# Kernel optimization log

Measured on AMD Instinct MI355X. Metric: run time of the kernel, lower is better.

Reference implementation:

```python
import jax, jax.numpy as jnp
import numpy as np

N_NODES = 100000
EPS = 1e-12  # F.normalize eps


def _sage_conv(x, src, dst, deg, Wl, bl, Wr):
    # mean aggregation of neighbor (source) features at destination nodes
    agg = jax.ops.segment_sum(x[src], dst, num_segments=N_NODES)  # [N, F]
    agg = agg / jnp.maximum(deg, 1.0)[:, None]
    out = agg @ Wl + bl + x @ Wr  # lin_l(mean(x_j)) + lin_r(x_i)
    # normalize=True -> L2 row normalization
    norm = jnp.sqrt(jnp.sum(out * out, axis=-1, keepdims=True))
    return out / jnp.maximum(norm, EPS)


def setup_inputs() -> dict:
    key = jax.random.key(0)
    ks = jax.random.split(key, 10)
    F_IN, H, C = 14, 32, 2
    x = jax.random.normal(ks[0], (N_NODES, F_IN), dtype=jnp.float32)
    edge_index = jax.random.randint(ks[1], (2, 6400000), 0, N_NODES, dtype=jnp.int32)
    def glorot(k, shape):
        lim = float(np.sqrt(6.0 / (shape[0] + shape[1])))
        return jax.random.uniform(k, shape, jnp.float32, -lim, lim)
    return {
        "x": x,
        "edge_index": edge_index,
        "W1l": glorot(ks[2], (F_IN, H)), "b1": jnp.zeros((H,), jnp.float32),
        "W1r": glorot(ks[3], (F_IN, H)),
        "W2l": glorot(ks[4], (H, H)), "b2": jnp.zeros((H,), jnp.float32),
        "W2r": glorot(ks[5], (H, H)),
        "Wlin": glorot(ks[6], (H, C)), "blin": jnp.zeros((C,), jnp.float32),
    }


def reference(x, edge_index, W1l, b1, W1r, W2l, b2, W2r, Wlin, blin):
    src, dst = edge_index[0], edge_index[1]
    deg = jax.ops.segment_sum(jnp.ones_like(dst, dtype=x.dtype), dst,
                              num_segments=N_NODES)  # in-degree per node
    h = jax.nn.relu(_sage_conv(x, src, dst, deg, W1l, b1, W1r))
    # dropout p=0.2 is identity at inference
    h = jax.nn.relu(_sage_conv(h, src, dst, deg, W2l, b2, W2r))
    return h @ Wlin + blin  # [N, num_classes]
```

## Files before the change

kernel.cpp:

```cpp
#include <hip/hip_runtime.h>
#include <hip/hip_bf16.h>


#define CHA 16384
#define MAXB 512
#define CAPB 18432
#define CAPH 9728
#define NPB 128

static __device__ __forceinline__ unsigned short f2bf(float f) {
    unsigned u = __float_as_uint(f);
    unsigned r = (u + 0x7FFFu + ((u >> 16) & 1u)) >> 16;
    return (unsigned short)r;
}
#define BF_LO(u) __uint_as_float((u) << 16)
#define BF_HI(u) __uint_as_float((u) & 0xFFFF0000u)

__global__ void cvt_x_bf16(const float* __restrict__ x, unsigned short* __restrict__ xb,
                           int* __restrict__ bcursor, int N, int NB) {
    int idx = blockIdx.x * blockDim.x + threadIdx.x;
    if (idx < NB) bcursor[idx] = idx * CAPB;
    if (idx >= N * 16) return;
    int n = idx >> 4, f = idx & 15;
    float v = (f < 14) ? x[n * 14 + f] : 0.f;
    xb[idx] = f2bf(v);
}

__global__ __launch_bounds__(1024) void partitionA(
        const int* __restrict__ src, const int* __restrict__ dst,
        int* __restrict__ bcursor, unsigned* __restrict__ part, int E, int NB) {
    __shared__ unsigned pk[CHA];
    __shared__ int h[MAXB], lofs[MAXB], cur[MAXB], delta[MAXB], tmp[MAXB];
    int t = threadIdx.x;
    int base = blockIdx.x * CHA;
    int end = base + CHA; if (end > E) end = E;
    int cnt = end - base;

    int ed[16], es[16];
    for (int i = t; i < NB; i += 1024) h[i] = 0;
    __syncthreads();
    #pragma unroll
    for (int i = 0; i < 4; ++i) {
        int j = i * 4096 + t * 4;
        if (j + 4 <= cnt) {
            int4 d4 = *(const int4*)(dst + base + j);
            int4 s4 = *(const int4*)(src + base + j);
            ed[i*4+0] = d4.x; ed[i*4+1] = d4.y; ed[i*4+2] = d4.z; ed[i*4+3] = d4.w;
            es[i*4+0] = s4.x; es[i*4+1] = s4.y; es[i*4+2] = s4.z; es[i*4+3] = s4.w;
            atomicAdd(&h[d4.x >> 8], 1);
            atomicAdd(&h[d4.y >> 8], 1);
            atomicAdd(&h[d4.z >> 8], 1);
            atomicAdd(&h[d4.w >> 8], 1);
        } else {
            #pragma unroll
            for (int k = 0; k < 4; ++k) {
                if (j + k < cnt) {
                    ed[i*4+k] = dst[base + j + k];
                    es[i*4+k] = src[base + j + k];
                    atomicAdd(&h[ed[i*4+k] >> 8], 1);
                } else ed[i*4+k] = -1;
            }
        }
    }
    __syncthreads();
    int v = 0;
    if (t < MAXB) { v = (t < NB) ? h[t] : 0; tmp[t] = v; }
    __syncthreads();
    for (int off = 1; off < MAXB; off <<= 1) {
        int a = 0;
        if (t < MAXB && t >= off) a = tmp[t - off];
        __syncthreads();
        if (t < MAXB) tmp[t] += a;
        __syncthreads();
    }
    if (t < NB) {
        int excl = tmp[t] - v;
        lofs[t] = excl;
        cur[t] = excl;
        int g = v ? atomicAdd(&bcursor[t], v) : 0;
        delta[t] = g - excl;
    }
    __syncthreads();
    #pragma unroll
    for (int i = 0; i < 16; ++i) {
        int d = ed[i];
        if (d >= 0) {
            int b = d >> 8;
            int r = atomicAdd(&cur[b], 1);
            pk[r] = ((unsigned)(d & 255) << 24) | (unsigned)es[i];
        }
    }
    __syncthreads();
    int wid = t >> 6, lane = t & 63;
    for (int b = wid; b < NB; b += 16) {
        int s = lofs[b];
        int e2 = (b + 1 < NB) ? lofs[b + 1] : cnt;
        int dlt = delta[b];
        int lim = (b + 1) * CAPB;
        for (int k = s + lane; k < e2; k += 64) {
            int gidx = dlt + k;
            if (gidx < lim) part[gidx] = pk[k];
        }
    }
}

__global__ __launch_bounds__(1024) void partitionB_fused(
        const unsigned* __restrict__ part, const int* __restrict__ bcursor,
        const uint4* __restrict__ xb4, const float* __restrict__ x,
        const float* __restrict__ W1l, const float* __restrict__ b1,
        const float* __restrict__ W1r,
        int* __restrict__ deg, int* __restrict__ offs, int* __restrict__ nlo,
        int* __restrict__ sorted_src, float* __restrict__ hbuf,
        unsigned short* __restrict__ hb, int N, int HALF) {
    __shared__ int pk2[CAPH];
    __shared__ int hh[256], tmp[256], keyofs[256];
    __shared__ int lstart[128], ldeg[128];
    __shared__ float sagg[128 * 17];
    __shared__ float sx[128 * 14];
    __shared__ float swl[448], swr[448], sb1[32];
    __shared__ int sTot;
    int b = blockIdx.x >> 1;
    int halfId = blockIdx.x & 1;
    int t = threadIdx.x;
    int start = b * CAPB;
    int end = bcursor[b];
    if (end > start + CAPB) end = start + CAPB;
    int rbase = blockIdx.x * CAPH;
    unsigned ce[18];
    if (t < 256) hh[t] = 0;
    if (t >= 512 && t < 960) { swl[t - 512] = W1l[t - 512]; swr[t - 512] = W1r[t - 512]; }
    else if (t >= 960 && t < 992) sb1[t - 960] = b1[t - 960];
    __syncthreads();
    #pragma unroll
    for (int i = 0; i < 18; ++i) {
        int idx = start + t + i * 1024;
        unsigned p = 0xFFFFFFFFu;
        if (idx < end) {
            p = part[idx];
            int dl = (int)(p >> 24);
            if ((dl >> 7) == halfId) {
                int key = (dl & 127) * 2 + (((int)(p & 0xFFFFFFu) < HALF) ? 0 : 1);
                atomicAdd(&hh[key], 1);
            } else p = 0xFFFFFFFFu;
        }
        ce[i] = p;
    }
    {
        int nbase = b * 256 + halfId * 128;
        int nnod = N - nbase; if (nnod > 128) nnod = 128; if (nnod < 0) nnod = 0;
        const float* gx = x + (size_t)nbase * 14;
        for (int i = t; i < nnod * 14; i += 1024) sx[i] = gx[i];
    }
    __syncthreads();
    int v = (t < 256) ? hh[t] : 0;
    if (t < 256) tmp[t] = v;
    __syncthreads();
    for (int off = 1; off < 256; off <<= 1) {
        int a2 = (t < 256 && t >= off) ? tmp[t - off] : 0;
        __syncthreads();
        if (t < 256) tmp[t] += a2;
        __syncthreads();
    }
    if (t < 256) keyofs[t] = tmp[t] - v;
    if (t == 255) sTot = tmp[255];
    __syncthreads();
    if (t < 128) {
        int lo = hh[2 * t];
        int d = lo + hh[2 * t + 1];
        int excl = keyofs[2 * t];
        lstart[t] = excl;
        ldeg[t] = d;
        int node = b * 256 + halfId * 128 + t;
        if (node < N) {
            deg[node] = d;
            offs[node] = rbase + excl;
            nlo[node] = lo;
        }
    }
    __syncthreads();
    #pragma unroll
    for (int i = 0; i < 18; ++i) {
        unsigned p = ce[i];
        if (p != 0xFFFFFFFFu) {
            int s = (int)(p & 0xFFFFFFu);
            int dl = (int)(p >> 24);
            int key = (dl & 127) * 2 + ((s < HALF) ? 0 : 1);
            int r = atomicAdd(&keyofs[key], 1);
            if (r < CAPH) pk2[r] = s;
        }
    }
    __syncthreads();
    int tot = sTot; if (tot > CAPH) tot = CAPH;
    for (int i = t; i < tot; i += 1024)
        sorted_src[rbase + i] = pk2[i];

    int node = t >> 3, sub = t & 7, ep = sub >> 1, half = sub & 1;
    int js = lstart[node], d = ldeg[node];
    int je = js + d;
    float a[8] = {0,0,0,0,0,0,0,0};
    int j = js + ep;
    for (; j + 4 < je; j += 8) {
        int s0 = pk2[j], s1 = pk2[j + 4];
        uint4 u0 = xb4[s0 * 2 + half], u1 = xb4[s1 * 2 + half];
        a[0] += BF_LO(u0.x) + BF_LO(u1.x);
        a[1] += BF_HI(u0.x) + BF_HI(u1.x);
        a[2] += BF_LO(u0.y) + BF_LO(u1.y);
        a[3] += BF_HI(u0.y) + BF_HI(u1.y);
        a[4] += BF_LO(u0.z) + BF_LO(u1.z);
        a[5] += BF_HI(u0.z) + BF_HI(u1.z);
        a[6] += BF_LO(u0.w) + BF_LO(u1.w);
        a[7] += BF_HI(u0.w) + BF_HI(u1.w);
    }
    for (; j < je; j += 4) {
        uint4 u0 = xb4[pk2[j] * 2 + half];
        a[0] += BF_LO(u0.x); a[1] += BF_HI(u0.x);
        a[2] += BF_LO(u0.y); a[3] += BF_HI(u0.y);
        a[4] += BF_LO(u0.z); a[5] += BF_HI(u0.z);
        a[6] += BF_LO(u0.w); a[7] += BF_HI(u0.w);
    }
    #pragma unroll
    for (int i = 0; i < 8; ++i) {
        a[i] += __shfl_xor(a[i], 2);
        a[i] += __shfl_xor(a[i], 4);
    }
    if (ep == 0) {
        #pragma unroll
        for (int i = 0; i < 8; ++i) sagg[node * 17 + half * 8 + i] = a[i];
    }
    __syncthreads();

    float inv = 1.0f / ((d > 0) ? (float)d : 1.0f);
    float acc[4];
    #pragma unroll
    for (int i = 0; i < 4; ++i) acc[i] = sb1[sub * 4 + i];
    #pragma unroll
    for (int k = 0; k < 14; ++k) {
        float ag = sagg[node * 17 + k] * inv;
        float xv = sx[node * 14 + k];
        float4 wl = *(const float4*)&swl[k * 32 + sub * 4];
        float4 wr = *(const float4*)&swr[k * 32 + sub * 4];
        acc[0] += ag * wl.x + xv * wr.x;
        acc[1] += ag * wl.y + xv * wr.y;
        acc[2] += ag * wl.z + xv * wr.z;
        acc[3] += ag * wl.w + xv * wr.w;
    }
    float ss = 0.f;
    #pragma unroll
    for (int i = 0; i < 4; ++i) ss += acc[i] * acc[i];
    ss += __shfl_xor(ss, 1); ss += __shfl_xor(ss, 2); ss += __shfl_xor(ss, 4);
    float invn = 1.f / fmaxf(sqrtf(ss), 1e-12f);
    int gnode = b * 256 + halfId * 128 + node;
    if (gnode < N) {
        float hv[4];
        #pragma unroll
        for (int i = 0; i < 4; ++i) hv[i] = fmaxf(acc[i] * invn, 0.f);
        *(float4*)(hbuf + (size_t)gnode * 32 + sub * 4) =
            make_float4(hv[0], hv[1], hv[2], hv[3]);
        uint2 pb;
        pb.x = (unsigned)f2bf(hv[0]) | ((unsigned)f2bf(hv[1]) << 16);
        pb.y = (unsigned)f2bf(hv[2]) | ((unsigned)f2bf(hv[3]) << 16);
        *(uint2*)(hb + (size_t)gnode * 32 + sub * 4) = pb;
    }
}

__global__ void gather32_p0(const uint4* __restrict__ hb, const int* __restrict__ sorted_src,
                            const int* __restrict__ offs, const int* __restrict__ nlo,
                            float4* __restrict__ agg2, int N) {
    int idx = blockIdx.x * blockDim.x + threadIdx.x;
    int n = idx >> 2;
    if (n >= N) return;
    int q = idx & 3;
    int start = offs[n];
    int jend = nlo[n];
    float a0=0,a1=0,a2=0,a3=0,a4=0,a5=0,a6=0,a7=0;
    int j = 0;
    for (; j + 4 <= jend; j += 4) {
        int s0 = sorted_src[start + j + 0];
        int s1 = sorted_src[start + j + 1];
        int s2 = sorted_src[start + j + 2];
        int s3 = sorted_src[start + j + 3];
        uint4 u0 = hb[s0 * 4 + q];
        uint4 u1 = hb[s1 * 4 + q];
        uint4 u2 = hb[s2 * 4 + q];
        uint4 u3 = hb[s3 * 4 + q];
        a0 += BF_LO(u0.x) + BF_LO(u1.x) + BF_LO(u2.x) + BF_LO(u3.x);
        a1 += BF_HI(u0.x) + BF_HI(u1.x) + BF_HI(u2.x) + BF_HI(u3.x);
        a2 += BF_LO(u0.y) + BF_LO(u1.y) + BF_LO(u2.y) + BF_LO(u3.y);
        a3 += BF_HI(u0.y) + BF_HI(u1.y) + BF_HI(u2.y) + BF_HI(u3.y);
        a4 += BF_LO(u0.z) + BF_LO(u1.z) + BF_LO(u2.z) + BF_LO(u3.z);
        a5 += BF_HI(u0.z) + BF_HI(u1.z) + BF_HI(u2.z) + BF_HI(u3.z);
        a6 += BF_LO(u0.w) + BF_LO(u1.w) + BF_LO(u2.w) + BF_LO(u3.w);
        a7 += BF_HI(u0.w) + BF_HI(u1.w) + BF_HI(u2.w) + BF_HI(u3.w);
    }
    for (; j < jend; ++j) {
        uint4 u0 = hb[sorted_src[start + j] * 4 + q];
        a0 += BF_LO(u0.x); a1 += BF_HI(u0.x);
        a2 += BF_LO(u0.y); a3 += BF_HI(u0.y);
        a4 += BF_LO(u0.z); a5 += BF_HI(u0.z);
        a6 += BF_LO(u0.w); a7 += BF_HI(u0.w);
    }
    agg2[n * 8 + q * 2 + 0] = make_float4(a0, a1, a2, a3);
    agg2[n * 8 + q * 2 + 1] = make_float4(a4, a5, a6, a7);
}

__global__ void gather32_p1(const uint4* __restrict__ hb, const int* __restrict__ sorted_src,
                            const int* __restrict__ offs, const int* __restrict__ deg,
                            const int* __restrict__ nlo, float4* __restrict__ agg2, int N) {
    int idx = blockIdx.x * blockDim.x + threadIdx.x;
    int n = idx >> 2;
    if (n >= N) return;
    int q = idx & 3;
    int start = offs[n];
    int d = deg[n];
    int j = nlo[n];
    float a0=0,a1=0,a2=0,a3=0,a4=0,a5=0,a6=0,a7=0;
    for (; j + 4 <= d; j += 4) {
        int s0 = sorted_src[start + j + 0];
        int s1 = sorted_src[start + j + 1];
        int s2 = sorted_src[start + j + 2];
        int s3 = sorted_src[start + j + 3];
        uint4 u0 = hb[s0 * 4 + q];
        uint4 u1 = hb[s1 * 4 + q];
        uint4 u2 = hb[s2 * 4 + q];
        uint4 u3 = hb[s3 * 4 + q];
        a0 += BF_LO(u0.x) + BF_LO(u1.x) + BF_LO(u2.x) + BF_LO(u3.x);
        a1 += BF_HI(u0.x) + BF_HI(u1.x) + BF_HI(u2.x) + BF_HI(u3.x);
        a2 += BF_LO(u0.y) + BF_LO(u1.y) + BF_LO(u2.y) + BF_LO(u3.y);
        a3 += BF_HI(u0.y) + BF_HI(u1.y) + BF_HI(u2.y) + BF_HI(u3.y);
        a4 += BF_LO(u0.z) + BF_LO(u1.z) + BF_LO(u2.z) + BF_LO(u3.z);
        a5 += BF_HI(u0.z) + BF_HI(u1.z) + BF_HI(u2.z) + BF_HI(u3.z);
        a6 += BF_LO(u0.w) + BF_LO(u1.w) + BF_LO(u2.w) + BF_LO(u3.w);
        a7 += BF_HI(u0.w) + BF_HI(u1.w) + BF_HI(u2.w) + BF_HI(u3.w);
    }
    for (; j < d; ++j) {
        uint4 u0 = hb[sorted_src[start + j] * 4 + q];
        a0 += BF_LO(u0.x); a1 += BF_HI(u0.x);
        a2 += BF_LO(u0.y); a3 += BF_HI(u0.y);
        a4 += BF_LO(u0.z); a5 += BF_HI(u0.z);
        a6 += BF_LO(u0.w); a7 += BF_HI(u0.w);
    }
    float inv = 1.0f / ((d > 0) ? (float)d : 1.0f);
    float4 p0 = agg2[n * 8 + q * 2 + 0];
    float4 p1 = agg2[n * 8 + q * 2 + 1];
    agg2[n * 8 + q * 2 + 0] = make_float4((p0.x + a0) * inv, (p0.y + a1) * inv,
                                          (p0.z + a2) * inv, (p0.w + a3) * inv);
    agg2[n * 8 + q * 2 + 1] = make_float4((p1.x + a4) * inv, (p1.y + a5) * inv,
                                          (p1.z + a6) * inv, (p1.w + a7) * inv);
}

__global__ __launch_bounds__(256) void dense2(
        const float* __restrict__ h, const float* __restrict__ agg2,
        const float* __restrict__ W2l, const float* __restrict__ b2,
        const float* __restrict__ W2r, const float* __restrict__ Wlin,
        const float* __restrict__ blin, float* __restrict__ out, int N) {
    __shared__ float sa[NPB * 33];
    __shared__ float sh2[NPB * 33];
    __shared__ float swl[32 * 32], swr[32 * 32], swo[64], sb[32], sbo[2];
    int t = threadIdx.x;
    int nb = blockIdx.x * NPB;
    int nn = N - nb; if (nn > NPB) nn = NPB;
    const float4* ga = (const float4*)(agg2 + (size_t)nb * 32);
    const float4* gh = (const float4*)(h + (size_t)nb * 32);
    for (int i = t; i < nn * 8; i += 256) {
        float4 v = ga[i];
        float* d = &sa[(i >> 3) * 33 + (i & 7) * 4];
        d[0] = v.x; d[1] = v.y; d[2] = v.z; d[3] = v.w;
        float4 w = gh[i];
        float* e = &sh2[(i >> 3) * 33 + (i & 7) * 4];
        e[0] = w.x; e[1] = w.y; e[2] = w.z; e[3] = w.w;
    }
    for (int i = t; i < 1024; i += 256) { swl[i] = W2l[i]; swr[i] = W2r[i]; }
    if (t < 64) swo[t] = Wlin[t];
    if (t < 32) sb[t] = b2[t];
    if (t < 2) sbo[t] = blin[t];
    __syncthreads();
    int q2 = t & 3;
    int p = t >> 2;
    int l0 = p * 2, l1 = l0 + 1;
    float acc0[8], acc1[8];
    #pragma unroll
    for (int j = 0; j < 8; ++j) { acc0[j] = sb[q2 * 8 + j]; acc1[j] = acc0[j]; }
    for (int k = 0; k < 32; ++k) {
        float a0 = sa[l0 * 33 + k],  a1 = sa[l1 * 33 + k];
        float h0 = sh2[l0 * 33 + k], h1 = sh2[l1 * 33 + k];
        const float4* wl4 = (const float4*)&swl[k * 32 + q2 * 8];
        const float4* wr4 = (const float4*)&swr[k * 32 + q2 * 8];
        float4 wla = wl4[0], wlb = wl4[1], wra = wr4[0], wrb = wr4[1];
        acc0[0] += a0 * wla.x + h0 * wra.x;  acc1[0] += a1 * wla.x + h1 * wra.x;
        acc0[1] += a0 * wla.y + h0 * wra.y;  acc1[1] += a1 * wla.y + h1 * wra.y;
        acc0[2] += a0 * wla.z + h0 * wra.z;  acc1[2] += a1 * wla.z + h1 * wra.z;
        acc0[3] += a0 * wla.w + h0 * wra.w;  acc1[3] += a1 * wla.w + h1 * wra.w;
        acc0[4] += a0 * wlb.x + h0 * wrb.x;  acc1[4] += a1 * wlb.x + h1 * wrb.x;
        acc0[5] += a0 * wlb.y + h0 * wrb.y;  acc1[5] += a1 * wlb.y + h1 * wrb.y;
        acc0[6] += a0 * wlb.z + h0 * wrb.z;  acc1[6] += a1 * wlb.z + h1 * wrb.z;
        acc0[7] += a0 * wlb.w + h0 * wrb.w;  acc1[7] += a1 * wlb.w + h1 * wrb.w;
    }
    float ss0 = 0.f, ss1 = 0.f;
    #pragma unroll
    for (int j = 0; j < 8; ++j) { ss0 += acc0[j] * acc0[j]; ss1 += acc1[j] * acc1[j]; }
    ss0 += __shfl_xor(ss0, 1); ss0 += __shfl_xor(ss0, 2);
    ss1 += __shfl_xor(ss1, 1); ss1 += __shfl_xor(ss1, 2);
    float inv0 = 1.f / fmaxf(sqrtf(ss0), 1e-12f);
    float inv1 = 1.f / fmaxf(sqrtf(ss1), 1e-12f);
    float o00 = 0.f, o01 = 0.f, o10 = 0.f, o11 = 0.f;
    #pragma unroll
    for (int j = 0; j < 8; ++j) {
        float hv0 = fmaxf(acc0[j] * inv0, 0.f);
        float hv1 = fmaxf(acc1[j] * inv1, 0.f);
        int kk = q2 * 8 + j;
        o00 += hv0 * swo[kk * 2 + 0];
        o01 += hv0 * swo[kk * 2 + 1];
        o10 += hv1 * swo[kk * 2 + 0];
        o11 += hv1 * swo[kk * 2 + 1];
    }
    o00 += __shfl_xor(o00, 1); o00 += __shfl_xor(o00, 2);
    o01 += __shfl_xor(o01, 1); o01 += __shfl_xor(o01, 2);
    o10 += __shfl_xor(o10, 1); o10 += __shfl_xor(o10, 2);
    o11 += __shfl_xor(o11, 1); o11 += __shfl_xor(o11, 2);
    if (q2 == 0) {
        int n0 = nb + l0, n1 = nb + l1;
        if (n0 < N) { out[n0 * 2 + 0] = o00 + sbo[0]; out[n0 * 2 + 1] = o01 + sbo[1]; }
        if (n1 < N) { out[n1 * 2 + 0] = o10 + sbo[0]; out[n1 * 2 + 1] = o11 + sbo[1]; }
    }
}

extern "C" void kernel_launch(void* const* d_in, const int* in_sizes, int n_in,
                              void* d_out, int out_size, void* d_ws, size_t ws_size,
                              hipStream_t stream) {
    const float* x    = (const float*)d_in[0];
    const int*   ei   = (const int*)d_in[1];
    const float* W1l  = (const float*)d_in[2];
    const float* b1   = (const float*)d_in[3];
    const float* W1r  = (const float*)d_in[4];
    const float* W2l  = (const float*)d_in[5];
    const float* b2   = (const float*)d_in[6];
    const float* W2r  = (const float*)d_in[7];
    const float* Wlin = (const float*)d_in[8];
    const float* blin = (const float*)d_in[9];
    float* out = (float*)d_out;

    const int N = in_sizes[0] / 14;
    const int E = in_sizes[1] / 2;
    const int* src = ei;
    const int* dst = ei + E;
    const int NB = (N + 255) / 256;
    const int HALF = N / 2;

    char* ws = (char*)d_ws;
    size_t off = 0;
    auto alloc = [&](size_t bytes) -> void* {
        void* p = ws + off;
        off = (off + bytes + 255) & ~(size_t)255;
        return p;
    };
    int*            bcursor    = (int*)alloc((size_t)NB * 4);
    unsigned*       part       = (unsigned*)alloc((size_t)NB * CAPB * 4);
    int*            sorted_src = (int*)alloc((size_t)NB * 2 * CAPH * 4);
    int*            deg        = (int*)alloc((size_t)N * 4);
    int*            offs       = (int*)alloc((size_t)N * 4);
    int*            nlo        = (int*)alloc((size_t)N * 4);
    unsigned short* xb         = (unsigned short*)alloc((size_t)N * 16 * 2);
    float*          hbuf       = (float*)alloc((size_t)N * 32 * 4);
    unsigned short* hb         = (unsigned short*)alloc((size_t)N * 32 * 2);
    float*          agg2       = (float*)part;
    (void)ws_size; (void)n_in; (void)out_size;

    cvt_x_bf16<<<(N * 16 + 255) / 256, 256, 0, stream>>>(x, xb, bcursor, N, NB);
    partitionA<<<(E + CHA - 1) / CHA, 1024, 0, stream>>>(src, dst, bcursor, part, E, NB);
    partitionB_fused<<<NB * 2, 1024, 0, stream>>>(
        part, bcursor, (const uint4*)xb, x, W1l, b1, W1r,
        deg, offs, nlo, sorted_src, hbuf, hb, N, HALF);
    gather32_p0<<<(N * 4 + 255) / 256, 256, 0, stream>>>(
        (const uint4*)hb, sorted_src, offs, nlo, (float4*)agg2, N);
    gather32_p1<<<(N * 4 + 255) / 256, 256, 0, stream>>>(
        (const uint4*)hb, sorted_src, offs, deg, nlo, (float4*)agg2, N);
    dense2<<<(N + NPB - 1) / NPB, 256, 0, stream>>>(
        hbuf, agg2, W2l, b2, W2r, Wlin, blin, out, N);
}
```

Before: 278.2 us.

## Partition edges into 128-node buckets directly, removing the half-bucket filter pass

The first partition pass now buckets edges by 128 destination nodes instead of 256, so the second pass reads only its own bucket. Before, each of two blocks read the whole 256-node bucket and discarded half the entries. This halves the part-buffer reads in partitionB and its per-thread register array. In exchange, partitionA keeps a larger shared histogram with a longer scan and writes to more, smaller buckets, which may scatter its global writes more.

```diff
diff --git a/kernel.cpp b/kernel.cpp
--- a/kernel.cpp
+++ b/kernel.cpp
@@ -3,8 +3,7 @@
 
 
 #define CHA 16384
-#define MAXB 512
-#define CAPB 18432
+#define MAXBH 800
 #define CAPH 9728
 #define NPB 128
 
@@ -17,9 +16,9 @@
 #define BF_HI(u) __uint_as_float((u) & 0xFFFF0000u)
 
 __global__ void cvt_x_bf16(const float* __restrict__ x, unsigned short* __restrict__ xb,
-                           int* __restrict__ bcursor, int N, int NB) {
+                           int* __restrict__ bcursor, int N, int NBH) {
     int idx = blockIdx.x * blockDim.x + threadIdx.x;
-    if (idx < NB) bcursor[idx] = idx * CAPB;
+    if (idx < NBH) bcursor[idx] = idx * CAPH;
     if (idx >= N * 16) return;
     int n = idx >> 4, f = idx & 15;
     float v = (f < 14) ? x[n * 14 + f] : 0.f;
@@ -28,16 +27,16 @@
 
 __global__ __launch_bounds__(1024) void partitionA(
         const int* __restrict__ src, const int* __restrict__ dst,
-        int* __restrict__ bcursor, unsigned* __restrict__ part, int E, int NB) {
+        int* __restrict__ bcursor, unsigned* __restrict__ part, int E, int NBH) {
     __shared__ unsigned pk[CHA];
-    __shared__ int h[MAXB], lofs[MAXB], cur[MAXB], delta[MAXB], tmp[MAXB];
+    __shared__ int h[MAXBH], lofs[MAXBH], cur[MAXBH], delta[MAXBH];
     int t = threadIdx.x;
     int base = blockIdx.x * CHA;
     int end = base + CHA; if (end > E) end = E;
     int cnt = end - base;
 
     int ed[16], es[16];
-    for (int i = t; i < NB; i += 1024) h[i] = 0;
+    for (int i = t; i < NBH; i += 1024) h[i] = 0;
     __syncthreads();
     #pragma unroll
     for (int i = 0; i < 4; ++i) {
@@ -47,34 +46,32 @@
             int4 s4 = *(const int4*)(src + base + j);
             ed[i*4+0] = d4.x; ed[i*4+1] = d4.y; ed[i*4+2] = d4.z; ed[i*4+3] = d4.w;
             es[i*4+0] = s4.x; es[i*4+1] = s4.y; es[i*4+2] = s4.z; es[i*4+3] = s4.w;
-            atomicAdd(&h[d4.x >> 8], 1);
-            atomicAdd(&h[d4.y >> 8], 1);
-            atomicAdd(&h[d4.z >> 8], 1);
-            atomicAdd(&h[d4.w >> 8], 1);
+            atomicAdd(&h[d4.x >> 7], 1);
+            atomicAdd(&h[d4.y >> 7], 1);
+            atomicAdd(&h[d4.z >> 7], 1);
+            atomicAdd(&h[d4.w >> 7], 1);
         } else {
             #pragma unroll
             for (int k = 0; k < 4; ++k) {
                 if (j + k < cnt) {
                     ed[i*4+k] = dst[base + j + k];
                     es[i*4+k] = src[base + j + k];
-                    atomicAdd(&h[ed[i*4+k] >> 8], 1);
+                    atomicAdd(&h[ed[i*4+k] >> 7], 1);
                 } else ed[i*4+k] = -1;
             }
         }
     }
     __syncthreads();
-    int v = 0;
-    if (t < MAXB) { v = (t < NB) ? h[t] : 0; tmp[t] = v; }
-    __syncthreads();
-    for (int off = 1; off < MAXB; off <<= 1) {
+    int v = (t < NBH) ? h[t] : 0;
+    for (int off = 1; off < MAXBH; off <<= 1) {
         int a = 0;
-        if (t < MAXB && t >= off) a = tmp[t - off];
+        if (t < NBH && t >= off) a = h[t - off];
         __syncthreads();
-        if (t < MAXB) tmp[t] += a;
+        if (t < NBH) h[t] += a;
         __syncthreads();
     }
-    if (t < NB) {
-        int excl = tmp[t] - v;
+    if (t < NBH) {
+        int excl = h[t] - v;
         lofs[t] = excl;
         cur[t] = excl;
         int g = v ? atomicAdd(&bcursor[t], v) : 0;
@@ -85,18 +82,18 @@
     for (int i = 0; i < 16; ++i) {
         int d = ed[i];
         if (d >= 0) {
-            int b = d >> 8;
+            int b = d >> 7;
             int r = atomicAdd(&cur[b], 1);
-            pk[r] = ((unsigned)(d & 255) << 24) | (unsigned)es[i];
+            pk[r] = ((unsigned)(d & 127) << 24) | (unsigned)es[i];
         }
     }
     __syncthreads();
     int wid = t >> 6, lane = t & 63;
-    for (int b = wid; b < NB; b += 16) {
+    for (int b = wid; b < NBH; b += 16) {
         int s = lofs[b];
-        int e2 = (b + 1 < NB) ? lofs[b + 1] : cnt;
+        int e2 = cur[b];
         int dlt = delta[b];
-        int lim = (b + 1) * CAPB;
+        int lim = (b + 1) * CAPH;
         for (int k = s + lane; k < e2; k += 64) {
             int gidx = dlt + k;
             if (gidx < lim) part[gidx] = pk[k];
@@ -119,34 +116,30 @@
     __shared__ float sx[128 * 14];
     __shared__ float swl[448], swr[448], sb1[32];
     __shared__ int sTot;
-    int b = blockIdx.x >> 1;
-    int halfId = blockIdx.x & 1;
+    int hbid = blockIdx.x;
     int t = threadIdx.x;
-    int start = b * CAPB;
-    int end = bcursor[b];
-    if (end > start + CAPB) end = start + CAPB;
-    int rbase = blockIdx.x * CAPH;
-    unsigned ce[18];
+    int start = hbid * CAPH;
+    int end = bcursor[hbid];
+    if (end > start + CAPH) end = start + CAPH;
+    int cnt = end - start;
+    unsigned ce[10];
     if (t < 256) hh[t] = 0;
     if (t >= 512 && t < 960) { swl[t - 512] = W1l[t - 512]; swr[t - 512] = W1r[t - 512]; }
     else if (t >= 960 && t < 992) sb1[t - 960] = b1[t - 960];
     __syncthreads();
     #pragma unroll
-    for (int i = 0; i < 18; ++i) {
+    for (int i = 0; i < 10; ++i) {
         int idx = start + t + i * 1024;
         unsigned p = 0xFFFFFFFFu;
         if (idx < end) {
             p = part[idx];
-            int dl = (int)(p >> 24);
-            if ((dl >> 7) == halfId) {
-                int key = (dl & 127) * 2 + (((int)(p & 0xFFFFFFu) < HALF) ? 0 : 1);
-                atomicAdd(&hh[key], 1);
-            } else p = 0xFFFFFFFFu;
+            int key = (int)(p >> 24) * 2 + (((int)(p & 0xFFFFFFu) < HALF) ? 0 : 1);
+            atomicAdd(&hh[key], 1);
         }
         ce[i] = p;
     }
     {
-        int nbase = b * 256 + halfId * 128;
+        int nbase = hbid * 128;
         int nnod = N - nbase; if (nnod > 128) nnod = 128; if (nnod < 0) nnod = 0;
         const float* gx = x + (size_t)nbase * 14;
         for (int i = t; i < nnod * 14; i += 1024) sx[i] = gx[i];
@@ -170,21 +163,20 @@
         int excl = keyofs[2 * t];
         lstart[t] = excl;
         ldeg[t] = d;
-        int node = b * 256 + halfId * 128 + t;
+        int node = hbid * 128 + t;
         if (node < N) {
             deg[node] = d;
-            offs[node] = rbase + excl;
+            offs[node] = start + excl;
             nlo[node] = lo;
         }
     }
     __syncthreads();
     #pragma unroll
-    for (int i = 0; i < 18; ++i) {
+    for (int i = 0; i < 10; ++i) {
         unsigned p = ce[i];
         if (p != 0xFFFFFFFFu) {
             int s = (int)(p & 0xFFFFFFu);
-            int dl = (int)(p >> 24);
-            int key = (dl & 127) * 2 + ((s < HALF) ? 0 : 1);
+            int key = (int)(p >> 24) * 2 + ((s < HALF) ? 0 : 1);
             int r = atomicAdd(&keyofs[key], 1);
             if (r < CAPH) pk2[r] = s;
         }
@@ -192,7 +184,7 @@
     __syncthreads();
     int tot = sTot; if (tot > CAPH) tot = CAPH;
     for (int i = t; i < tot; i += 1024)
-        sorted_src[rbase + i] = pk2[i];
+        sorted_src[start + i] = pk2[i];
 
     int node = t >> 3, sub = t & 7, ep = sub >> 1, half = sub & 1;
     int js = lstart[node], d = ldeg[node];
@@ -249,7 +241,7 @@
     for (int i = 0; i < 4; ++i) ss += acc[i] * acc[i];
     ss += __shfl_xor(ss, 1); ss += __shfl_xor(ss, 2); ss += __shfl_xor(ss, 4);
     float invn = 1.f / fmaxf(sqrtf(ss), 1e-12f);
-    int gnode = b * 256 + halfId * 128 + node;
+    int gnode = hbid * 128 + node;
     if (gnode < N) {
         float hv[4];
         #pragma unroll
@@ -443,7 +435,7 @@
     const int E = in_sizes[1] / 2;
     const int* src = ei;
     const int* dst = ei + E;
-    const int NB = (N + 255) / 256;
+    const int NBH = (N + 127) / 128;
     const int HALF = N / 2;
 
     char* ws = (char*)d_ws;
@@ -453,9 +445,9 @@
         off = (off + bytes + 255) & ~(size_t)255;
         return p;
     };
-    int*            bcursor    = (int*)alloc((size_t)NB * 4);
-    unsigned*       part       = (unsigned*)alloc((size_t)NB * CAPB * 4);
-    int*            sorted_src = (int*)alloc((size_t)NB * 2 * CAPH * 4);
+    int*            bcursor    = (int*)alloc((size_t)NBH * 4);
+    unsigned*       part       = (unsigned*)alloc((size_t)NBH * CAPH * 4);
+    int*            sorted_src = (int*)alloc((size_t)NBH * CAPH * 4);
     int*            deg        = (int*)alloc((size_t)N * 4);
     int*            offs       = (int*)alloc((size_t)N * 4);
     int*            nlo        = (int*)alloc((size_t)N * 4);
@@ -465,9 +457,9 @@
     float*          agg2       = (float*)part;
     (void)ws_size; (void)n_in; (void)out_size;
 
-    cvt_x_bf16<<<(N * 16 + 255) / 256, 256, 0, stream>>>(x, xb, bcursor, N, NB);
-    partitionA<<<(E + CHA - 1) / CHA, 1024, 0, stream>>>(src, dst, bcursor, part, E, NB);
-    partitionB_fused<<<NB * 2, 1024, 0, stream>>>(
+    cvt_x_bf16<<<(N * 16 + 255) / 256, 256, 0, stream>>>(x, xb, bcursor, N, NBH);
+    partitionA<<<(E + CHA - 1) / CHA, 1024, 0, stream>>>(src, dst, bcursor, part, E, NBH);
+    partitionB_fused<<<NBH, 1024, 0, stream>>>(
         part, bcursor, (const uint4*)xb, x, W1l, b1, W1r,
         deg, offs, nlo, sorted_src, hbuf, hb, N, HALF);
     gather32_p0<<<(N * 4 + 255) / 256, 256, 0, stream>>>(
```

New measurement: 276.1 us. No clear change (-0.7%).
